# Performance work log

Measured on AMD Instinct MI355X. Metric: run time of the kernel, lower is better.

The kernel has to match this reference:

```python
import jax, jax.numpy as jnp
import numpy as np

N = 10000   # num_nodes (batch=1)
E = 160000  # num edges
CIN, H, T, OUT, K = 32, 64, 12, 12, 3


def _conv1d(x, w, b, pad):
    # x: [N, C_in, T], w: [C_out, C_in, K]
    out = jax.lax.conv_general_dilated(
        x, w, window_strides=(1,), padding=[(pad, pad)],
        dimension_numbers=('NCH', 'OIH', 'NCH'))
    return out + b[None, :, None]


def _gated_tconv(x, w, b):
    # GatedTemporalConv (dropout = identity in eval)
    out = _conv1d(x, w, b, K // 2)
    P, Q = jnp.split(out, 2, axis=1)
    return P * jax.nn.sigmoid(Q)


def _gcn(x, W, b, src, dst, ew):
    # PyG GCNConv, vectorized over all T timesteps in one fused pass.
    # x: [N, C_in, T], W: [C_out, C_in]
    xt = jnp.einsum('nct,oc->not', x, W)
    loop = jnp.arange(N)
    srcl = jnp.concatenate([src, loop])
    dstl = jnp.concatenate([dst, loop])
    ewl = jnp.concatenate([ew, jnp.ones((N,), ew.dtype)])
    deg = jax.ops.segment_sum(ewl, dstl, num_segments=N)
    dis = jnp.where(deg > 0, jax.lax.rsqrt(deg), 0.0)
    norm = dis[srcl] * ewl * dis[dstl]                      # [E+N]
    msg = xt[srcl] * norm[:, None, None]                    # [E+N, C_out, T]
    out = jax.ops.segment_sum(msg, dstl, num_segments=N)    # [N, C_out, T]
    return out + b[None, :, None]


def setup_inputs() -> dict:
    key = jax.random.key(0)
    ks = jax.random.split(key, 20)
    rn = lambda k, s: jax.random.normal(k, s, jnp.float32) * 0.05
    return {
        'x': jax.random.normal(ks[0], (N, CIN, T), jnp.float32),
        'edge_index': jax.random.randint(ks[1], (2, E), 0, N),
        'edge_weight': jax.random.uniform(ks[2], (E,), jnp.float32),
        'tc1a_w': rn(ks[3], (2 * H, CIN, K)), 'tc1a_b': rn(ks[4], (2 * H,)),
        'gc1_w': rn(ks[5], (H, H)),           'gc1_b': rn(ks[6], (H,)),
        'tc1b_w': rn(ks[7], (2 * H, H, K)),   'tc1b_b': rn(ks[8], (2 * H,)),
        'tc2a_w': rn(ks[9], (2 * H, H, K)),   'tc2a_b': rn(ks[10], (2 * H,)),
        'gc2_w': rn(ks[11], (H, H)),          'gc2_b': rn(ks[12], (H,)),
        'tc2b_w': rn(ks[13], (2 * H, H, K)),  'tc2b_b': rn(ks[14], (2 * H,)),
        'fin_w': rn(ks[15], (OUT, H, T)),     'fin_b': rn(ks[16], (OUT,)),
    }


def reference(x, edge_index, edge_weight,
              tc1a_w, tc1a_b, gc1_w, gc1_b, tc1b_w, tc1b_b,
              tc2a_w, tc2a_b, gc2_w, gc2_b, tc2b_w, tc2b_b,
              fin_w, fin_b):
    src, dst = edge_index[0], edge_index[1]
    h = _gated_tconv(x, tc1a_w, tc1a_b)
    h = jax.nn.relu(_gcn(h, gc1_w, gc1_b, src, dst, edge_weight))
    h = _gated_tconv(h, tc1b_w, tc1b_b)
    h = _gated_tconv(h, tc2a_w, tc2a_b)
    h = jax.nn.relu(_gcn(h, gc2_w, gc2_b, src, dst, edge_weight))
    h = _gated_tconv(h, tc2b_w, tc2b_b)
    h = _conv1d(h, fin_w, fin_b, 0)          # [N, OUT, 1] (kernel == T)
    h = h[:, :, 0]                            # squeeze(-1)
    return h.reshape(1, N, OUT)               # batch_size = 1
```

## Files before the change

kernel.cpp:

```cpp
#include <hip/hip_runtime.h>
#include <hip/hip_bf16.h>
#include <stdint.h>

#define N_NODES 10000
#define N_EDGES 160000
#define BUCKET 128
#define UNROLL_SLOTS 24

typedef unsigned short u16;
typedef unsigned int u32;
typedef short s16v8 __attribute__((ext_vector_type(8)));
typedef float f32v4 __attribute__((ext_vector_type(4)));
typedef float f32v2 __attribute__((ext_vector_type(2)));
typedef unsigned int u32v4 __attribute__((ext_vector_type(4)));
typedef unsigned int u32v2 __attribute__((ext_vector_type(2)));

__device__ __forceinline__ float bf2f(u16 v){ return __uint_as_float(((u32)v) << 16); }
__device__ __forceinline__ u16 f2bf(float f){
    u32 u = __float_as_uint(f);
    u32 r = (u + 0x7fffu + ((u >> 16) & 1u)) >> 16;
    return (u16)r;
}
__device__ __forceinline__ f32v2 up2(u32 v){
    f32v2 r;
    r.x = __uint_as_float(v << 16);
    r.y = __uint_as_float(v & 0xffff0000u);
    return r;
}
__device__ __forceinline__ u32 pk2(float lo, float hi){
    return (u32)f2bf(lo) | ((u32)f2bf(hi) << 16);
}

struct SmallPtrs { const void* p[14]; };

__device__ __constant__ const int g_seg_off[15] = {
    0, 12288, 12416, 16512, 16576, 41152, 41280,
    65856, 65984, 70080, 70144, 94720, 94848, 104064, 104076
};
__device__ __constant__ const int g_seg_kind[14] = {
    1, 0, 0, 0, 2, 0, 2, 0, 0, 0, 2, 0, 0, 0
};

__global__ void k_convert_init(SmallPtrs ps, u16* __restrict__ dst,
                               float* deg, int* cur){
    int i = blockIdx.x * blockDim.x + threadIdx.x;
    if (i < 104076){
        int seg = 0, base = 0;
#pragma unroll
        for (int s = 0; s < 14; s++){
            if (i >= g_seg_off[s]){ seg = s; base = g_seg_off[s]; }
        }
        int li = i - base;
        float v = ((const float*)ps.p[seg])[li];
        int kind = g_seg_kind[seg];
        int dsto = li;
        if (kind){
            int CIN = (kind == 1) ? 32 : 64;
            int o = li / (3 * CIN);
            int rem = li - o * (3 * CIN);
            int c = rem / 3, d = rem - c * 3;
            dsto = d * 128 * CIN + o * CIN + c;
        }
        dst[base + dsto] = f2bf(v);
    }
    if (i < N_NODES){ deg[i] = 1.0f; cur[i] = 0; }
}

__launch_bounds__(256, 4)
__global__ void k_gconv_count(const float* __restrict__ xin, const u16* __restrict__ wg,
                              const u16* __restrict__ bg, u16* __restrict__ out,
                              const int* __restrict__ ei, const float* __restrict__ ew,
                              float* deg, int* cur, int2* __restrict__ epack){
    if (blockIdx.x >= 1250){
        int e = (blockIdx.x - 1250) * 256 + threadIdx.x;
        if (e < N_EDGES){
            int s = ei[e];
            int d = ei[N_EDGES + e];
            float wv = ew[e];
            atomicAdd(&deg[d], wv);
            int p = atomicAdd(&cur[d], 1);
            if (p < BUCKET) epack[d * BUCKET + p] = make_int2(s, __float_as_int(wv));
        }
        return;
    }
    __shared__ __attribute__((aligned(16))) u16 shbuf[6912];
    u16* xT = shbuf;
    u16* Ho = shbuf;
    int tid = threadIdx.x;
    int n0 = blockIdx.x * 8;

    int lane = tid & 63, wave = tid >> 6;
    int col = lane & 15, quad = lane >> 4;
    int o_p = wave * 16 + col, o_q = o_p + 64;

    s16v8 Bf[3][2];
#pragma unroll
    for (int pq = 0; pq < 2; pq++){
        int o = pq ? o_q : o_p;
#pragma unroll
        for (int d = 0; d < 3; d++)
            Bf[d][pq] = *(const s16v8*)(wg + d * 4096 + o * 32 + quad * 8);
    }

    for (int i = tid; i < 8 * 40; i += 256){
        int g = i / 40, c = i % 40;
        xT[g * 560 + 0 * 40 + c] = 0; xT[g * 560 + 13 * 40 + c] = 0;
    }
    {
        int g = tid >> 5, c = tid & 31;
        const float4* p = (const float4*)(xin + ((size_t)(n0 + g) * 32 + c) * 12);
        float4 v0 = p[0], v1 = p[1], v2 = p[2];
        u16* xb = xT + g * 560 + c;
        xb[1 * 40] = f2bf(v0.x);  xb[2 * 40] = f2bf(v0.y);
        xb[3 * 40] = f2bf(v0.z);  xb[4 * 40] = f2bf(v0.w);
        xb[5 * 40] = f2bf(v1.x);  xb[6 * 40] = f2bf(v1.y);
        xb[7 * 40] = f2bf(v1.z);  xb[8 * 40] = f2bf(v1.w);
        xb[9 * 40] = f2bf(v2.x);  xb[10 * 40] = f2bf(v2.y);
        xb[11 * 40] = f2bf(v2.z); xb[12 * 40] = f2bf(v2.w);
    }
    __syncthreads();

    f32v4 aP[6], aQ[6];
#pragma unroll
    for (int mt = 0; mt < 6; mt++){ aP[mt] = (f32v4)0.f; aQ[mt] = (f32v4)0.f; }
#pragma unroll
    for (int mt = 0; mt < 6; mt++){
        int m = mt * 16 + col;
        int g = m / 12, t = m - 12 * g;
#pragma unroll
        for (int d = 0; d < 3; d++){
            s16v8 a = *(const s16v8*)&xT[g * 560 + (t + d) * 40 + quad * 8];
            aP[mt] = __builtin_amdgcn_mfma_f32_16x16x32_bf16(a, Bf[d][0], aP[mt], 0, 0, 0);
            aQ[mt] = __builtin_amdgcn_mfma_f32_16x16x32_bf16(a, Bf[d][1], aQ[mt], 0, 0, 0);
        }
    }
    __syncthreads();
    float bP = bf2f(bg[o_p]), bQ = bf2f(bg[o_q]);
#pragma unroll
    for (int mt = 0; mt < 6; mt++){
#pragma unroll
        for (int r = 0; r < 4; r++){
            int m2 = mt * 16 + quad * 4 + r;
            int g = m2 / 12, t = m2 - 12 * g;
            float pv = aP[mt][r] + bP, qv = aQ[mt][r] + bQ;
            Ho[g * 864 + t * 72 + o_p] = f2bf(pv / (1.f + __expf(-qv)));
        }
    }
    __syncthreads();
    for (int i = tid; i < 768; i += 256){
        int g = i / 96, r = i % 96, t = r / 8, ch = r % 8;
        *(s16v8*)(out + (size_t)(n0 + g) * 768 + t * 64 + ch * 8) =
            *(const s16v8*)&Ho[g * 864 + t * 72 + ch * 8];
    }
}

__global__ void k_norm(const float* __restrict__ deg, const int* __restrict__ cur,
                       int2* __restrict__ ep){
    int i = blockIdx.x * blockDim.x + threadIdx.x;
    int n = i >> 7, slot = i & 127;
    if (n >= N_NODES) return;
    int cnt = cur[n]; if (cnt > BUCKET) cnt = BUCKET;
    if (slot < cnt){
        int2 e = ep[(size_t)n * BUCKET + slot];
        float w = __int_as_float(e.y) * rsqrtf(deg[e.x]) * rsqrtf(deg[n]);
        ep[(size_t)n * BUCKET + slot].y = __float_as_int(w);
    } else if (slot < UNROLL_SLOTS){
        ep[(size_t)n * BUCKET + slot] = make_int2(0, 0);
    }
}

#define XIDX(g, row, c) (((g) * 14 + (row)) * 72 + (c))

#define GFMA(W, A0, A1, A2) { \
    acc[0]  += (W) * up2((A0).x); acc[1]  += (W) * up2((A0).y); \
    acc[2]  += (W) * up2((A0).z); acc[3]  += (W) * up2((A0).w); \
    acc[4]  += (W) * up2((A1).x); acc[5]  += (W) * up2((A1).y); \
    acc[6]  += (W) * up2((A1).z); acc[7]  += (W) * up2((A1).w); \
    acc[8]  += (W) * up2((A2).x); acc[9]  += (W) * up2((A2).y); \
    acc[10] += (W) * up2((A2).z); acc[11] += (W) * up2((A2).w); }

#define GPAIR(P) { \
    int4 m = *(const int4*)(eb + (P)); \
    const u16* q0 = src + (size_t)(u32)m.x * 768 + fo; \
    const u16* q1 = src + (size_t)(u32)m.z * 768 + fo; \
    u32v4 a0 = *(const u32v4*)(q0); \
    u32v4 a1 = *(const u32v4*)(q0 + 256); \
    u32v4 a2 = *(const u32v4*)(q0 + 512); \
    u32v4 c0 = *(const u32v4*)(q1); \
    u32v4 c1 = *(const u32v4*)(q1 + 256); \
    u32v4 c2 = *(const u32v4*)(q1 + 512); \
    f32v2 w0; w0.x = __int_as_float(m.y); w0.y = w0.x; \
    f32v2 w1; w1.x = __int_as_float(m.w); w1.y = w1.x; \
    GFMA(w0, a0, a1, a2); \
    GFMA(w1, c0, c1, c2); }

#define GSINGLE(P) { \
    int2 e0 = eb[(P)]; \
    const u16* q0 = src + (size_t)(u32)e0.x * 768 + fo; \
    u32v4 a0 = *(const u32v4*)(q0); \
    u32v4 a1 = *(const u32v4*)(q0 + 256); \
    u32v4 a2 = *(const u32v4*)(q0 + 512); \
    f32v2 w0; w0.x = __int_as_float(e0.y); w0.y = w0.x; \
    GFMA(w0, a0, a1, a2); }

template<bool LAST>
__launch_bounds__(256, 4)
__global__ void k_gfused(const u16* __restrict__ src,
                         const float* __restrict__ deg, const int* __restrict__ cur,
                         const int2* __restrict__ ep,
                         const u16* __restrict__ Wmix, const u16* __restrict__ bmix,
                         const u16* __restrict__ w1, const u16* __restrict__ b1,
                         const u16* __restrict__ w2, const u16* __restrict__ b2,
                         const u16* __restrict__ fw, const u16* __restrict__ fb,
                         u16* __restrict__ outMid, float* __restrict__ outFin){
    __shared__ __attribute__((aligned(16))) u16 bufX[8 * 14 * 72];
    __shared__ __attribute__((aligned(16))) u16 bufY[8 * 14 * 72];
    int tid = threadIdx.x;
    int n0 = blockIdx.x * 8;
    int lane = tid & 63, wave = tid >> 6;
    int col = lane & 15, quad = lane >> 4;
    int o_p = wave * 16 + col, o_q = o_p + 64;

    for (int i = tid; i < 8 * 72; i += 256){
        int g = i / 72, c = i % 72;
        bufX[XIDX(g, 0, c)] = 0; bufX[XIDX(g, 13, c)] = 0;
        bufY[XIDX(g, 0, c)] = 0; bufY[XIDX(g, 13, c)] = 0;
    }

    {
        int nl = tid >> 5;
        int l  = tid & 31;
        int n  = n0 + nl;
        int fo = l * 8;
        int e = cur[n]; if (e > BUCKET) e = BUCKET;

        f32v2 acc[12];
        {
            float sw = 1.0f / deg[n];
            f32v2 swv; swv.x = sw; swv.y = sw;
            const u16* q = src + (size_t)n * 768 + fo;
            u32v4 s0 = *(const u32v4*)(q);
            u32v4 s1 = *(const u32v4*)(q + 256);
            u32v4 s2 = *(const u32v4*)(q + 512);
            acc[0]  = swv * up2(s0.x); acc[1]  = swv * up2(s0.y);
            acc[2]  = swv * up2(s0.z); acc[3]  = swv * up2(s0.w);
            acc[4]  = swv * up2(s1.x); acc[5]  = swv * up2(s1.y);
            acc[6]  = swv * up2(s1.z); acc[7]  = swv * up2(s1.w);
            acc[8]  = swv * up2(s2.x); acc[9]  = swv * up2(s2.y);
            acc[10] = swv * up2(s2.z); acc[11] = swv * up2(s2.w);
        }

        const int2* eb = ep + (size_t)n * BUCKET;
        GPAIR(0);  GPAIR(2);  GPAIR(4);  GPAIR(6);
        GPAIR(8);  GPAIR(10); GPAIR(12); GPAIR(14);
        GPAIR(16); GPAIR(18); GPAIR(20); GPAIR(22);

        if (e > UNROLL_SLOTS){
            int p = UNROLL_SLOTS;
            for (; p + 1 < e; p += 2) GPAIR(p);
            if (p < e) GSINGLE(p);
        }

#pragma unroll
        for (int gi = 0; gi < 3; gi++){
            int f0 = gi * 256 + fo;
            int t = f0 >> 6, c = f0 & 63;
            u32v4 hv;
            hv.x = pk2(acc[4 * gi + 0].x, acc[4 * gi + 0].y);
            hv.y = pk2(acc[4 * gi + 1].x, acc[4 * gi + 1].y);
            hv.z = pk2(acc[4 * gi + 2].x, acc[4 * gi + 2].y);
            hv.w = pk2(acc[4 * gi + 3].x, acc[4 * gi + 3].y);
            *(u32v4*)&bufX[XIDX(nl, 1 + t, c)] = hv;
        }
    }
    __syncthreads();

    {
        f32v4 accm[6];
#pragma unroll
        for (int mt = 0; mt < 6; mt++) accm[mt] = (f32v4)0.f;
#pragma unroll
        for (int ks = 0; ks < 2; ks++){
            s16v8 Bm = *(const s16v8*)(Wmix + (size_t)o_p * 64 + ks * 32 + quad * 8);
#pragma unroll
            for (int mt = 0; mt < 6; mt++){
                int m = mt * 16 + col;
                int g = m / 12, t = m - 12 * g;
                s16v8 a = *(const s16v8*)&bufX[XIDX(g, 1 + t, ks * 32 + quad * 8)];
                accm[mt] = __builtin_amdgcn_mfma_f32_16x16x32_bf16(a, Bm, accm[mt], 0, 0, 0);
            }
        }
        float bm = bf2f(bmix[o_p]);
#pragma unroll
        for (int mt = 0; mt < 6; mt++){
#pragma unroll
            for (int r = 0; r < 4; r++){
                int m2 = mt * 16 + quad * 4 + r;
                int g = m2 / 12, t = m2 - 12 * g;
                bufY[XIDX(g, 1 + t, o_p)] = f2bf(fmaxf(accm[mt][r] + bm, 0.f));
            }
        }
    }
    __syncthreads();

    {
        f32v4 aP[6], aQ[6];
#pragma unroll
        for (int mt = 0; mt < 6; mt++){ aP[mt] = (f32v4)0.f; aQ[mt] = (f32v4)0.f; }
#pragma unroll
        for (int ks = 0; ks < 2; ks++){
            s16v8 Bf[3][2];
#pragma unroll
            for (int pq = 0; pq < 2; pq++){
                int o = pq ? o_q : o_p;
#pragma unroll
                for (int d = 0; d < 3; d++)
                    Bf[d][pq] = *(const s16v8*)(w1 + d * 8192 + o * 64 + ks * 32 + quad * 8);
            }
#pragma unroll
            for (int mt = 0; mt < 6; mt++){
                int m = mt * 16 + col;
                int g = m / 12, t = m - 12 * g;
#pragma unroll
                for (int d = 0; d < 3; d++){
                    s16v8 a = *(const s16v8*)&bufY[XIDX(g, t + d, ks * 32 + quad * 8)];
                    aP[mt] = __builtin_amdgcn_mfma_f32_16x16x32_bf16(a, Bf[d][0], aP[mt], 0, 0, 0);
                    aQ[mt] = __builtin_amdgcn_mfma_f32_16x16x32_bf16(a, Bf[d][1], aQ[mt], 0, 0, 0);
                }
            }
        }
        float bP = bf2f(b1[o_p]), bQ = bf2f(b1[o_q]);
#pragma unroll
        for (int mt = 0; mt < 6; mt++){
#pragma unroll
            for (int r = 0; r < 4; r++){
                int m2 = mt * 16 + quad * 4 + r;
                int g = m2 / 12, t = m2 - 12 * g;
                float pv = aP[mt][r] + bP, qv = aQ[mt][r] + bQ;
                u16 hv = f2bf(pv / (1.f + __expf(-qv)));
                if (LAST) bufX[g * 1008 + o_p * 12 + t] = hv;
                else      bufX[XIDX(g, 1 + t, o_p)] = hv;
            }
        }
    }
    __syncthreads();

    if (!LAST){
        f32v4 aP[6], aQ[6];
#pragma unroll
        for (int mt = 0; mt < 6; mt++){ aP[mt] = (f32v4)0.f; aQ[mt] = (f32v4)0.f; }
#pragma unroll
        for (int ks = 0; ks < 2; ks++){
            s16v8 Bf[3][2];
#pragma unroll
            for (int pq = 0; pq < 2; pq++){
                int o = pq ? o_q : o_p;
#pragma unroll
                for (int d = 0; d < 3; d++)
                    Bf[d][pq] = *(const s16v8*)(w2 + d * 8192 + o * 64 + ks * 32 + quad * 8);
            }
#pragma unroll
            for (int mt = 0; mt < 6; mt++){
                int m = mt * 16 + col;
                int g = m / 12, t = m - 12 * g;
#pragma unroll
                for (int d = 0; d < 3; d++){
                    s16v8 a = *(const s16v8*)&bufX[XIDX(g, t + d, ks * 32 + quad * 8)];
                    aP[mt] = __builtin_amdgcn_mfma_f32_16x16x32_bf16(a, Bf[d][0], aP[mt], 0, 0, 0);
                    aQ[mt] = __builtin_amdgcn_mfma_f32_16x16x32_bf16(a, Bf[d][1], aQ[mt], 0, 0, 0);
                }
            }
        }
        float bP = bf2f(b2[o_p]), bQ = bf2f(b2[o_q]);
#pragma unroll
        for (int mt = 0; mt < 6; mt++){
#pragma unroll
            for (int r = 0; r < 4; r++){
                int m2 = mt * 16 + quad * 4 + r;
                int g = m2 / 12, t = m2 - 12 * g;
                float pv = aP[mt][r] + bP, qv = aQ[mt][r] + bQ;
                bufY[XIDX(g, 1 + t, o_p)] = f2bf(pv / (1.f + __expf(-qv)));
            }
        }
        __syncthreads();
        for (int i = tid; i < 768; i += 256){
            int g = i / 96, r = i % 96, t = r / 8, ch = r % 8;
            *(s16v8*)(outMid + (size_t)(n0 + g) * 768 + t * 64 + ch * 8) =
                *(const s16v8*)&bufY[XIDX(g, 1 + t, ch * 8)];
        }
    } else {
        if (wave == 0){
            f32v4 accF = {0.f, 0.f, 0.f, 0.f};
            int g8 = col & 7;
#pragma unroll
            for (int ks = 0; ks < 24; ks++){
                s16v8 a = *(const s16v8*)&bufX[g8 * 1008 + ks * 32 + quad * 8];
                s16v8 bfr = {0, 0, 0, 0, 0, 0, 0, 0};
                if (col < 12)
                    bfr = *(const s16v8*)(fw + (size_t)col * 768 + ks * 32 + quad * 8);
                accF = __builtin_amdgcn_mfma_f32_16x16x32_bf16(a, bfr, accF, 0, 0, 0);
            }
            if (col < 12 && quad < 2){
                float bb = bf2f(fb[col]);
#pragma unroll
                for (int r = 0; r < 4; r++){
                    int g = quad * 4 + r;
                    outFin[(size_t)(n0 + g) * 12 + col] = accF[r] + bb;
                }
            }
        }
    }
}

static inline size_t align256(size_t x){ return (x + 255) & ~(size_t)255; }

extern "C" void kernel_launch(void* const* d_in, const int* in_sizes, int n_in,
                              void* d_out, int out_size, void* d_ws, size_t ws_size,
                              hipStream_t stream){
    const float* x  = (const float*)d_in[0];
    const int* ei   = (const int*)d_in[1];
    const float* ew = (const float*)d_in[2];

    char* w = (char*)d_ws;
    u16* bufA    = (u16*)w;  w += align256((size_t)N_NODES * 768 * sizeof(u16));
    u16* bufB    = (u16*)w;  w += align256((size_t)N_NODES * 768 * sizeof(u16));
    float* deg   = (float*)w; w += align256(N_NODES * sizeof(float));
    int* cur     = (int*)w;   w += align256(N_NODES * sizeof(int));
    int2* epack  = (int2*)w;  w += align256((size_t)N_NODES * BUCKET * sizeof(int2));
    u16* cvt     = (u16*)w;   w += align256(104076 * sizeof(u16));

    u16* tc1a_w = cvt + 0;
    u16* tc1a_b = cvt + 12288;
    u16* gc1_w  = cvt + 12416;
    u16* gc1_b  = cvt + 16512;
    u16* tc1b_w = cvt + 16576;
    u16* tc1b_b = cvt + 41152;
    u16* tc2a_w = cvt + 41280;
    u16* tc2a_b = cvt + 65856;
    u16* gc2_w  = cvt + 65984;
    u16* gc2_b  = cvt + 70080;
    u16* tc2b_w = cvt + 70144;
    u16* tc2b_b = cvt + 94720;
    u16* fin_w  = cvt + 94848;
    u16* fin_b  = cvt + 104064;

    SmallPtrs ps;
    ps.p[0]  = d_in[3];  ps.p[1]  = d_in[4];
    ps.p[2]  = d_in[5];  ps.p[3]  = d_in[6];
    ps.p[4]  = d_in[7];  ps.p[5]  = d_in[8];
    ps.p[6]  = d_in[9];  ps.p[7]  = d_in[10];
    ps.p[8]  = d_in[11]; ps.p[9]  = d_in[12];
    ps.p[10] = d_in[13]; ps.p[11] = d_in[14];
    ps.p[12] = d_in[15]; ps.p[13] = d_in[16];

    k_convert_init<<<(104076 + 255) / 256, 256, 0, stream>>>(ps, cvt, deg, cur);
    k_gconv_count<<<1250 + 625, 256, 0, stream>>>(x, tc1a_w, tc1a_b, bufA, ei, ew, deg, cur, epack);
    k_norm<<<(N_NODES * BUCKET) / 256, 256, 0, stream>>>(deg, cur, epack);

    k_gfused<false><<<1250, 256, 0, stream>>>(bufA, deg, cur, epack,
                                              gc1_w, gc1_b, tc1b_w, tc1b_b,
                                              tc2a_w, tc2a_b, nullptr, nullptr,
                                              bufB, nullptr);
    k_gfused<true><<<1250, 256, 0, stream>>>(bufB, deg, cur, epack,
                                             gc2_w, gc2_b, tc2b_w, tc2b_b,
                                             nullptr, nullptr, fin_w, fin_b,
                                             nullptr, (float*)d_out);
}
```

Baseline: 225.4 us.

## Split edge gather across two thread groups per node, halve nodes per block

```diff
diff --git a/kernel.cpp b/kernel.cpp
--- a/kernel.cpp
+++ b/kernel.cpp
@@ -169,7 +169,8 @@
     }
 }
 
-#define XIDX(g, row, c) (((g) * 14 + (row)) * 72 + (c))
+#define XIDX(g, row, c) ((g) * 1008 + (row) * 72 + (c))
+#define YIDX(g, row, c) (4032 + (g) * 1008 + (row) * 72 + (c))
 
 #define GFMA(W, A0, A1, A2) { \
     acc[0]  += (W) * up2((A0).x); acc[1]  += (W) * up2((A0).y); \
@@ -204,7 +205,7 @@
     GFMA(w0, a0, a1, a2); }
 
 template<bool LAST>
-__launch_bounds__(256, 4)
+__launch_bounds__(256, 6)
 __global__ void k_gfused(const u16* __restrict__ src,
                          const float* __restrict__ deg, const int* __restrict__ cur,
                          const int2* __restrict__ ep,
@@ -213,29 +214,25 @@
                          const u16* __restrict__ w2, const u16* __restrict__ b2,
                          const u16* __restrict__ fw, const u16* __restrict__ fb,
                          u16* __restrict__ outMid, float* __restrict__ outFin){
-    __shared__ __attribute__((aligned(16))) u16 bufX[8 * 14 * 72];
-    __shared__ __attribute__((aligned(16))) u16 bufY[8 * 14 * 72];
+    __shared__ __attribute__((aligned(16))) u16 shmem[8064];
     int tid = threadIdx.x;
-    int n0 = blockIdx.x * 8;
+    int n0 = blockIdx.x * 4;
     int lane = tid & 63, wave = tid >> 6;
     int col = lane & 15, quad = lane >> 4;
     int o_p = wave * 16 + col, o_q = o_p + 64;
 
-    for (int i = tid; i < 8 * 72; i += 256){
-        int g = i / 72, c = i % 72;
-        bufX[XIDX(g, 0, c)] = 0; bufX[XIDX(g, 13, c)] = 0;
-        bufY[XIDX(g, 0, c)] = 0; bufY[XIDX(g, 13, c)] = 0;
-    }
-
     {
-        int nl = tid >> 5;
+        int grp = tid >> 7;
+        int nl = (tid >> 5) & 3;
         int l  = tid & 31;
         int n  = n0 + nl;
         int fo = l * 8;
-        int e = cur[n]; if (e > BUCKET) e = BUCKET;
+        const int2* eb = ep + (size_t)n * BUCKET;
+        float* S = (float*)shmem;
+        int sbase = nl * 768 + l * 4;
 
         f32v2 acc[12];
-        {
+        if (grp == 0){
             float sw = 1.0f / deg[n];
             f32v2 swv; swv.x = sw; swv.y = sw;
             const u16* q = src + (size_t)n * 768 + fo;
@@ -248,65 +245,97 @@
             acc[6]  = swv * up2(s1.z); acc[7]  = swv * up2(s1.w);
             acc[8]  = swv * up2(s2.x); acc[9]  = swv * up2(s2.y);
             acc[10] = swv * up2(s2.z); acc[11] = swv * up2(s2.w);
-        }
-
-        const int2* eb = ep + (size_t)n * BUCKET;
-        GPAIR(0);  GPAIR(2);  GPAIR(4);  GPAIR(6);
-        GPAIR(8);  GPAIR(10); GPAIR(12); GPAIR(14);
-        GPAIR(16); GPAIR(18); GPAIR(20); GPAIR(22);
-
-        if (e > UNROLL_SLOTS){
-            int p = UNROLL_SLOTS;
-            for (; p + 1 < e; p += 2) GPAIR(p);
-            if (p < e) GSINGLE(p);
-        }
-
-#pragma unroll
-        for (int gi = 0; gi < 3; gi++){
-            int f0 = gi * 256 + fo;
-            int t = f0 >> 6, c = f0 & 63;
-            u32v4 hv;
-            hv.x = pk2(acc[4 * gi + 0].x, acc[4 * gi + 0].y);
-            hv.y = pk2(acc[4 * gi + 1].x, acc[4 * gi + 1].y);
-            hv.z = pk2(acc[4 * gi + 2].x, acc[4 * gi + 2].y);
-            hv.w = pk2(acc[4 * gi + 3].x, acc[4 * gi + 3].y);
-            *(u32v4*)&bufX[XIDX(nl, 1 + t, c)] = hv;
+            GPAIR(0); GPAIR(2); GPAIR(4); GPAIR(6); GPAIR(8); GPAIR(10);
+#pragma unroll
+            for (int gi = 0; gi < 3; gi++){
+                f32v4 h0, h1;
+                h0.x = acc[4 * gi + 0].x; h0.y = acc[4 * gi + 0].y;
+                h0.z = acc[4 * gi + 1].x; h0.w = acc[4 * gi + 1].y;
+                h1.x = acc[4 * gi + 2].x; h1.y = acc[4 * gi + 2].y;
+                h1.z = acc[4 * gi + 3].x; h1.w = acc[4 * gi + 3].y;
+                *(f32v4*)&S[sbase + gi * 256]       = h0;
+                *(f32v4*)&S[sbase + gi * 256 + 128] = h1;
+            }
+        } else {
+#pragma unroll
+            for (int k = 0; k < 12; k++) acc[k] = (f32v2)0.f;
+            int e = cur[n]; if (e > BUCKET) e = BUCKET;
+            GPAIR(12); GPAIR(14); GPAIR(16); GPAIR(18); GPAIR(20); GPAIR(22);
+            if (e > UNROLL_SLOTS){
+                int p = UNROLL_SLOTS;
+                for (; p + 1 < e; p += 2) GPAIR(p);
+                if (p < e) GSINGLE(p);
+            }
+        }
+        __syncthreads();
+        if (grp == 1){
+#pragma unroll
+            for (int gi = 0; gi < 3; gi++){
+                f32v4 h0 = *(const f32v4*)&S[sbase + gi * 256];
+                f32v4 h1 = *(const f32v4*)&S[sbase + gi * 256 + 128];
+                acc[4 * gi + 0].x += h0.x; acc[4 * gi + 0].y += h0.y;
+                acc[4 * gi + 1].x += h0.z; acc[4 * gi + 1].y += h0.w;
+                acc[4 * gi + 2].x += h1.x; acc[4 * gi + 2].y += h1.y;
+                acc[4 * gi + 3].x += h1.z; acc[4 * gi + 3].y += h1.w;
+            }
+        }
+        __syncthreads();
+        if (grp == 1){
+#pragma unroll
+            for (int gi = 0; gi < 3; gi++){
+                int f0 = gi * 256 + fo;
+                int t = f0 >> 6, c = f0 & 63;
+                u32v4 hv;
+                hv.x = pk2(acc[4 * gi + 0].x, acc[4 * gi + 0].y);
+                hv.y = pk2(acc[4 * gi + 1].x, acc[4 * gi + 1].y);
+                hv.z = pk2(acc[4 * gi + 2].x, acc[4 * gi + 2].y);
+                hv.w = pk2(acc[4 * gi + 3].x, acc[4 * gi + 3].y);
+                *(u32v4*)&shmem[YIDX(nl, 1 + t, c)] = hv;
+            }
+        } else {
+            for (int i = tid; i < 576; i += 128){
+                int g = i / 144, rem = i % 144;
+                int row = (rem < 72) ? 0 : 13;
+                int c = rem % 72;
+                shmem[XIDX(g, row, c)] = 0;
+                shmem[YIDX(g, row, c)] = 0;
+            }
         }
     }
     __syncthreads();
 
     {
-        f32v4 accm[6];
-#pragma unroll
-        for (int mt = 0; mt < 6; mt++) accm[mt] = (f32v4)0.f;
+        f32v4 accm[3];
+#pragma unroll
+        for (int mt = 0; mt < 3; mt++) accm[mt] = (f32v4)0.f;
 #pragma unroll
         for (int ks = 0; ks < 2; ks++){
             s16v8 Bm = *(const s16v8*)(Wmix + (size_t)o_p * 64 + ks * 32 + quad * 8);
 #pragma unroll
-            for (int mt = 0; mt < 6; mt++){
+            for (int mt = 0; mt < 3; mt++){
                 int m = mt * 16 + col;
                 int g = m / 12, t = m - 12 * g;
-                s16v8 a = *(const s16v8*)&bufX[XIDX(g, 1 + t, ks * 32 + quad * 8)];
+                s16v8 a = *(const s16v8*)&shmem[YIDX(g, 1 + t, ks * 32 + quad * 8)];
                 accm[mt] = __builtin_amdgcn_mfma_f32_16x16x32_bf16(a, Bm, accm[mt], 0, 0, 0);
             }
         }
         float bm = bf2f(bmix[o_p]);
 #pragma unroll
-        for (int mt = 0; mt < 6; mt++){
+        for (int mt = 0; mt < 3; mt++){
 #pragma unroll
             for (int r = 0; r < 4; r++){
                 int m2 = mt * 16 + quad * 4 + r;
                 int g = m2 / 12, t = m2 - 12 * g;
-                bufY[XIDX(g, 1 + t, o_p)] = f2bf(fmaxf(accm[mt][r] + bm, 0.f));
+                shmem[XIDX(g, 1 + t, o_p)] = f2bf(fmaxf(accm[mt][r] + bm, 0.f));
             }
         }
     }
     __syncthreads();
 
     {
-        f32v4 aP[6], aQ[6];
-#pragma unroll
-        for (int mt = 0; mt < 6; mt++){ aP[mt] = (f32v4)0.f; aQ[mt] = (f32v4)0.f; }
+        f32v4 aP[3], aQ[3];
+#pragma unroll
+        for (int mt = 0; mt < 3; mt++){ aP[mt] = (f32v4)0.f; aQ[mt] = (f32v4)0.f; }
 #pragma unroll
         for (int ks = 0; ks < 2; ks++){
             s16v8 Bf[3][2];
@@ -318,12 +347,12 @@
                     Bf[d][pq] = *(const s16v8*)(w1 + d * 8192 + o * 64 + ks * 32 + quad * 8);
             }
 #pragma unroll
-            for (int mt = 0; mt < 6; mt++){
+            for (int mt = 0; mt < 3; mt++){
                 int m = mt * 16 + col;
                 int g = m / 12, t = m - 12 * g;
 #pragma unroll
                 for (int d = 0; d < 3; d++){
-                    s16v8 a = *(const s16v8*)&bufY[XIDX(g, t + d, ks * 32 + quad * 8)];
+                    s16v8 a = *(const s16v8*)&shmem[XIDX(g, t + d, ks * 32 + quad * 8)];
                     aP[mt] = __builtin_amdgcn_mfma_f32_16x16x32_bf16(a, Bf[d][0], aP[mt], 0, 0, 0);
                     aQ[mt] = __builtin_amdgcn_mfma_f32_16x16x32_bf16(a, Bf[d][1], aQ[mt], 0, 0, 0);
                 }
@@ -331,24 +360,24 @@
         }
         float bP = bf2f(b1[o_p]), bQ = bf2f(b1[o_q]);
 #pragma unroll
-        for (int mt = 0; mt < 6; mt++){
+        for (int mt = 0; mt < 3; mt++){
 #pragma unroll
             for (int r = 0; r < 4; r++){
                 int m2 = mt * 16 + quad * 4 + r;
                 int g = m2 / 12, t = m2 - 12 * g;
                 float pv = aP[mt][r] + bP, qv = aQ[mt][r] + bQ;
                 u16 hv = f2bf(pv / (1.f + __expf(-qv)));
-                if (LAST) bufX[g * 1008 + o_p * 12 + t] = hv;
-                else      bufX[XIDX(g, 1 + t, o_p)] = hv;
+                if (LAST) shmem[4032 + g * 1008 + o_p * 12 + t] = hv;
+                else      shmem[YIDX(g, 1 + t, o_p)] = hv;
             }
         }
     }
     __syncthreads();
 
     if (!LAST){
-        f32v4 aP[6], aQ[6];
-#pragma unroll
-        for (int mt = 0; mt < 6; mt++){ aP[mt] = (f32v4)0.f; aQ[mt] = (f32v4)0.f; }
+        f32v4 aP[3], aQ[3];
+#pragma unroll
+        for (int mt = 0; mt < 3; mt++){ aP[mt] = (f32v4)0.f; aQ[mt] = (f32v4)0.f; }
 #pragma unroll
         for (int ks = 0; ks < 2; ks++){
             s16v8 Bf[3][2];
@@ -360,12 +389,12 @@
                     Bf[d][pq] = *(const s16v8*)(w2 + d * 8192 + o * 64 + ks * 32 + quad * 8);
             }
 #pragma unroll
-            for (int mt = 0; mt < 6; mt++){
+            for (int mt = 0; mt < 3; mt++){
                 int m = mt * 16 + col;
                 int g = m / 12, t = m - 12 * g;
 #pragma unroll
                 for (int d = 0; d < 3; d++){
-                    s16v8 a = *(const s16v8*)&bufX[XIDX(g, t + d, ks * 32 + quad * 8)];
+                    s16v8 a = *(const s16v8*)&shmem[YIDX(g, t + d, ks * 32 + quad * 8)];
                     aP[mt] = __builtin_amdgcn_mfma_f32_16x16x32_bf16(a, Bf[d][0], aP[mt], 0, 0, 0);
                     aQ[mt] = __builtin_amdgcn_mfma_f32_16x16x32_bf16(a, Bf[d][1], aQ[mt], 0, 0, 0);
                 }
@@ -373,39 +402,38 @@
         }
         float bP = bf2f(b2[o_p]), bQ = bf2f(b2[o_q]);
 #pragma unroll
-        for (int mt = 0; mt < 6; mt++){
+        for (int mt = 0; mt < 3; mt++){
 #pragma unroll
             for (int r = 0; r < 4; r++){
                 int m2 = mt * 16 + quad * 4 + r;
                 int g = m2 / 12, t = m2 - 12 * g;
                 float pv = aP[mt][r] + bP, qv = aQ[mt][r] + bQ;
-                bufY[XIDX(g, 1 + t, o_p)] = f2bf(pv / (1.f + __expf(-qv)));
+                shmem[XIDX(g, 1 + t, o_p)] = f2bf(pv / (1.f + __expf(-qv)));
             }
         }
         __syncthreads();
-        for (int i = tid; i < 768; i += 256){
-            int g = i / 96, r = i % 96, t = r / 8, ch = r % 8;
+        for (int i = tid; i < 384; i += 256){
+            int g = i / 96, r = i % 96, t = r >> 3, ch = r & 7;
             *(s16v8*)(outMid + (size_t)(n0 + g) * 768 + t * 64 + ch * 8) =
-                *(const s16v8*)&bufY[XIDX(g, 1 + t, ch * 8)];
+                *(const s16v8*)&shmem[XIDX(g, 1 + t, ch * 8)];
         }
     } else {
         if (wave == 0){
             f32v4 accF = {0.f, 0.f, 0.f, 0.f};
-            int g8 = col & 7;
+            int g4 = col & 3;
 #pragma unroll
             for (int ks = 0; ks < 24; ks++){
-                s16v8 a = *(const s16v8*)&bufX[g8 * 1008 + ks * 32 + quad * 8];
+                s16v8 a = *(const s16v8*)&shmem[4032 + g4 * 1008 + ks * 32 + quad * 8];
                 s16v8 bfr = {0, 0, 0, 0, 0, 0, 0, 0};
                 if (col < 12)
                     bfr = *(const s16v8*)(fw + (size_t)col * 768 + ks * 32 + quad * 8);
                 accF = __builtin_amdgcn_mfma_f32_16x16x32_bf16(a, bfr, accF, 0, 0, 0);
             }
-            if (col < 12 && quad < 2){
+            if (col < 12 && quad == 0){
                 float bb = bf2f(fb[col]);
 #pragma unroll
                 for (int r = 0; r < 4; r++){
-                    int g = quad * 4 + r;
-                    outFin[(size_t)(n0 + g) * 12 + col] = accF[r] + bb;
+                    outFin[(size_t)(n0 + r) * 12 + col] = accF[r] + bb;
                 }
             }
         }
@@ -457,11 +485,11 @@
     k_gconv_count<<<1250 + 625, 256, 0, stream>>>(x, tc1a_w, tc1a_b, bufA, ei, ew, deg, cur, epack);
     k_norm<<<(N_NODES * BUCKET) / 256, 256, 0, stream>>>(deg, cur, epack);
 
-    k_gfused<false><<<1250, 256, 0, stream>>>(bufA, deg, cur, epack,
+    k_gfused<false><<<2500, 256, 0, stream>>>(bufA, deg, cur, epack,
                                               gc1_w, gc1_b, tc1b_w, tc1b_b,
                                               tc2a_w, tc2a_b, nullptr, nullptr,
                                               bufB, nullptr);
-    k_gfused<true><<<1250, 256, 0, stream>>>(bufB, deg, cur, epack,
+    k_gfused<true><<<2500, 256, 0, stream>>>(bufB, deg, cur, epack,
                                              gc2_w, gc2_b, tc2b_w, tc2b_b,
                                              nullptr, nullptr, fin_w, fin_b,
                                              nullptr, (float*)d_out);
```

After: 229.4 us. About the same (+1.7%).
